# Kernel optimization log

Measured on AMD Instinct MI355X. Metric: run time of the kernel, lower is better.

Reference implementation:

```python
import jax, jax.numpy as jnp
import numpy as np

N_NODES = 100000
N_EDGES = 1600000
D = 128
L = 3
BN_EPS = 1e-5


def setup_inputs() -> dict:
    key = jax.random.key(0)
    ks = jax.random.split(key, 6)
    x = jax.random.normal(ks[0], (N_NODES, D), dtype=jnp.float32)
    edge_index = jax.random.randint(ks[1], (2, N_EDGES), 0, N_NODES, dtype=jnp.int64)
    Wl = jax.random.normal(ks[2], (L, D, D), dtype=jnp.float32) / np.sqrt(D)
    bl = jax.random.normal(ks[3], (L, D), dtype=jnp.float32) * 0.01
    Wr = jax.random.normal(ks[4], (L, D, D), dtype=jnp.float32) / np.sqrt(D)
    gamma = jnp.ones((L, D), dtype=jnp.float32)
    beta = jnp.zeros((L, D), dtype=jnp.float32)
    return {"x": x, "edge_index": edge_index, "Wl": Wl, "bl": bl,
            "Wr": Wr, "gamma": gamma, "beta": beta}


def _sage_layer(x, src, dst, inv_deg, Wl_i, bl_i, Wr_i, gamma_i, beta_i):
    # mean aggregation over incoming edges: scatter-add messages then divide by degree
    agg_sum = jax.ops.segment_sum(x[src], dst, num_segments=N_NODES)  # [N, D]
    agg = agg_sum * inv_deg[:, None]
    # SAGEConv: lin_l(agg) (with bias) + lin_r(x) (no bias)
    h = jnp.einsum('nd,hd->nh', agg, Wl_i) + bl_i + jnp.einsum('nd,hd->nh', x, Wr_i)
    # BatchNorm1d (training-mode batch stats, biased variance)
    mean = jnp.mean(h, axis=0)
    var = jnp.mean(jnp.square(h - mean), axis=0)
    h = (h - mean) * jax.lax.rsqrt(var + BN_EPS) * gamma_i + beta_i
    return jax.nn.relu(h)  # dropout is identity in eval mode


def reference(x, edge_index, Wl, bl, Wr, gamma, beta):
    src, dst = edge_index[0], edge_index[1]
    deg = jax.ops.segment_sum(jnp.ones((N_EDGES,), jnp.float32), dst,
                              num_segments=N_NODES)
    inv_deg = 1.0 / jnp.maximum(deg, 1.0)
    for i in range(L):
        h = _sage_layer(x, src, dst, inv_deg, Wl[i], bl[i], Wr[i], gamma[i], beta[i])
        if 0 < i < L - 1:  # middle layers get a scaled residual (shapes match)
            x = x + 0.5 * h
        else:
            x = h
    return x
```

## Files before the change

kernel.cpp:

```cpp
#include <hip/hip_runtime.h>

#define N_NODES 100000
#define N_EDGES 1600000
#define D 128
#define BN_EPS 1e-5f
#define N_GB ((N_NODES + 63) / 64)
#define NPART 8
#define FILL_BLOCKS 2048
#define NODES_PER_PART (N_NODES / NPART)
#define CAP 80

typedef short bf16x8 __attribute__((ext_vector_type(8)));
typedef float f32x4 __attribute__((ext_vector_type(4)));

__device__ inline unsigned short f32_to_bf16_rne(float f) {
    unsigned u = __builtin_bit_cast(unsigned, f);
    u += 0x7fffu + ((u >> 16) & 1u);
    return (unsigned short)(u >> 16);
}
__device__ inline float bf16lo_to_f32(unsigned v) { return __builtin_bit_cast(float, v << 16); }
__device__ inline float bf16hi_to_f32(unsigned v) { return __builtin_bit_cast(float, v & 0xffff0000u); }

__device__ inline void gload_lds16(const void* g, void* l) {
    __builtin_amdgcn_global_load_lds((const __attribute__((address_space(1))) unsigned*)g,
                                     (__attribute__((address_space(3))) unsigned*)l, 16, 0, 0);
}


__global__ __launch_bounds__(256) void k_prep(const float* __restrict__ x_in,
                                              const float* __restrict__ Wl, const float* __restrict__ Wr,
                                              unsigned short* __restrict__ xhi,
                                              unsigned short* __restrict__ wl_hi, unsigned short* __restrict__ wl_lo,
                                              unsigned short* __restrict__ wr_hi, unsigned short* __restrict__ wr_lo) {
    for (int idx = blockIdx.x * 256 + threadIdx.x; idx < N_NODES * 32; idx += FILL_BLOCKS * 256) {
        float4 v = ((const float4*)x_in)[idx];
        uint2 p;
        p.x = (unsigned)f32_to_bf16_rne(v.x) | ((unsigned)f32_to_bf16_rne(v.y) << 16);
        p.y = (unsigned)f32_to_bf16_rne(v.z) | ((unsigned)f32_to_bf16_rne(v.w) << 16);
        ((uint2*)xhi)[idx] = p;
    }
    for (int i = blockIdx.x * 256 + threadIdx.x; i < 2 * 3 * D * D; i += FILL_BLOCKS * 256) {
        const float* srcp = (i < 3 * D * D) ? Wl : Wr;
        int j = (i < 3 * D * D) ? i : i - 3 * D * D;
        float w = srcp[j];
        unsigned short h = f32_to_bf16_rne(w);
        float rem = w - bf16lo_to_f32((unsigned)h);
        if (i < 3 * D * D) { wl_hi[j] = h; wl_lo[j] = f32_to_bf16_rne(rem); }
        else               { wr_hi[j] = h; wr_lo[j] = f32_to_bf16_rne(rem); }
    }
}

__global__ __launch_bounds__(256) void k_fill(const int* __restrict__ src, const int* __restrict__ dst,
                                              int* __restrict__ cursor, int* __restrict__ colidx) {
    const int part = blockIdx.x & (NPART - 1);
    const int lo = part * NODES_PER_PART;
    const int hi = lo + NODES_PER_PART;
    const int stride = (FILL_BLOCKS / NPART) * 256;
    for (int e = (blockIdx.x >> 3) * 256 + threadIdx.x; e < N_EDGES; e += stride) {
        int d = dst[e];
        if (d >= lo && d < hi) {
            int pos = atomicAdd(&cursor[d], 1);
            if (pos < CAP) colidx[d * CAP + pos] = src[e];
        }
    }
}


__global__ __launch_bounds__(256) void k_agg(const unsigned short* __restrict__ xhi,
                                             const int* __restrict__ cursor, const int* __restrict__ colidx,
                                             unsigned short* __restrict__ agghi) {
    const int wid = threadIdx.x >> 6;
    const int l = threadIdx.x & 63;
    const int n = blockIdx.x * 4 + wid;
    if (n >= N_NODES) return;
    const int degree = cursor[n];
    const int b = n * CAP;
    const int e = b + (degree < CAP ? degree : CAP);
    const int c8 = l & 15;
    const int g = l >> 4;
    const size_t coff = (size_t)c8 * 16;

    float acc[8];
#pragma unroll
    for (int k = 0; k < 8; k++) acc[k] = 0.f;

    int i = b;
    while (i < e) {
        int chunk = e - i; if (chunk > 64) chunk = 64;
        int myE = colidx[i + (l < chunk ? l : chunk - 1)];
        int j = 0;
        for (; j + 8 <= chunk; j += 8) {
            int s0 = __shfl(myE, j + g);
            int s1 = __shfl(myE, j + 4 + g);
            uint4 v0 = *(const uint4*)((const char*)xhi + (size_t)s0 * 256 + coff);
            uint4 v1 = *(const uint4*)((const char*)xhi + (size_t)s1 * 256 + coff);
            acc[0] += bf16lo_to_f32(v0.x); acc[1] += bf16hi_to_f32(v0.x);
            acc[2] += bf16lo_to_f32(v0.y); acc[3] += bf16hi_to_f32(v0.y);
            acc[4] += bf16lo_to_f32(v0.z); acc[5] += bf16hi_to_f32(v0.z);
            acc[6] += bf16lo_to_f32(v0.w); acc[7] += bf16hi_to_f32(v0.w);
            acc[0] += bf16lo_to_f32(v1.x); acc[1] += bf16hi_to_f32(v1.x);
            acc[2] += bf16lo_to_f32(v1.y); acc[3] += bf16hi_to_f32(v1.y);
            acc[4] += bf16lo_to_f32(v1.z); acc[5] += bf16hi_to_f32(v1.z);
            acc[6] += bf16lo_to_f32(v1.w); acc[7] += bf16hi_to_f32(v1.w);
        }
        for (; j + 4 <= chunk; j += 4) {
            int s0 = __shfl(myE, j + g);
            uint4 v0 = *(const uint4*)((const char*)xhi + (size_t)s0 * 256 + coff);
            acc[0] += bf16lo_to_f32(v0.x); acc[1] += bf16hi_to_f32(v0.x);
            acc[2] += bf16lo_to_f32(v0.y); acc[3] += bf16hi_to_f32(v0.y);
            acc[4] += bf16lo_to_f32(v0.z); acc[5] += bf16hi_to_f32(v0.z);
            acc[6] += bf16lo_to_f32(v0.w); acc[7] += bf16hi_to_f32(v0.w);
        }
        if (j < chunk) {
            int idx = j + g;
            int s0 = __shfl(myE, idx < chunk ? idx : chunk - 1);
            if (idx < chunk) {
                uint4 v0 = *(const uint4*)((const char*)xhi + (size_t)s0 * 256 + coff);
                acc[0] += bf16lo_to_f32(v0.x); acc[1] += bf16hi_to_f32(v0.x);
                acc[2] += bf16lo_to_f32(v0.y); acc[3] += bf16hi_to_f32(v0.y);
                acc[4] += bf16lo_to_f32(v0.z); acc[5] += bf16hi_to_f32(v0.z);
                acc[6] += bf16lo_to_f32(v0.w); acc[7] += bf16hi_to_f32(v0.w);
            }
        }
        i += chunk;
    }
#pragma unroll
    for (int k = 0; k < 8; k++) {
        acc[k] += __shfl_xor(acc[k], 16);
        acc[k] += __shfl_xor(acc[k], 32);
    }
    if (g == 0) {
        float idg = 1.0f / fmaxf((float)degree, 1.0f);
        uint4 p;
        p.x = (unsigned)f32_to_bf16_rne(acc[0] * idg) | ((unsigned)f32_to_bf16_rne(acc[1] * idg) << 16);
        p.y = (unsigned)f32_to_bf16_rne(acc[2] * idg) | ((unsigned)f32_to_bf16_rne(acc[3] * idg) << 16);
        p.z = (unsigned)f32_to_bf16_rne(acc[4] * idg) | ((unsigned)f32_to_bf16_rne(acc[5] * idg) << 16);
        p.w = (unsigned)f32_to_bf16_rne(acc[6] * idg) | ((unsigned)f32_to_bf16_rne(acc[7] * idg) << 16);
        *(uint4*)((char*)agghi + (size_t)n * 256 + coff) = p;
    }
}

__global__ __launch_bounds__(256, 2) void k_gemm(
    const unsigned short* __restrict__ agg_hi, const unsigned short* __restrict__ x_hi,
    const unsigned short* __restrict__ wl_hi, const unsigned short* __restrict__ wl_lo,
    const unsigned short* __restrict__ wr_hi, const unsigned short* __restrict__ wr_lo,
    const float* __restrict__ bl, unsigned short* __restrict__ h, float* __restrict__ partial) {
    __shared__ char lds[32768];
    const int t = threadIdx.x;
    const int w = t >> 6;
    const int l = t & 63;
    const int lr = l & 15;
    const int lg = l >> 4;
    const int base = blockIdx.x * 64;
    const int j0 = w * 32;

    {
#pragma unroll
        for (int i = 0; i < 8; i++) {
            int c = w * 8 + i;
            int ci = c & 15;
            int m = ci >> 2, kk = ci & 3;
            int n = base + m * 16 + lr;
            if (n > N_NODES - 1) n = N_NODES - 1;
            size_t goff = (size_t)n * 256 + kk * 64 + lg * 16;
            const char* srcp = ((c & 16) ? (const char*)x_hi : (const char*)agg_hi) + goff;
            gload_lds16(srcp, lds + c * 1024);
        }
    }

    f32x4 acc[4][2];
#pragma unroll
    for (int m = 0; m < 4; m++)
#pragma unroll
        for (int f = 0; f < 2; f++) acc[m][f] = (f32x4){0.f, 0.f, 0.f, 0.f};

#pragma unroll
    for (int seg = 0; seg < 2; seg++) {
        const unsigned short* WH = seg ? wr_hi : wl_hi;
        const unsigned short* WLo = seg ? wr_lo : wl_lo;
        bf16x8 wh[4][2], wlo[4][2];
#pragma unroll
        for (int kk = 0; kk < 4; kk++)
#pragma unroll
            for (int f = 0; f < 2; f++) {
                size_t wo = (size_t)(j0 + f * 16 + lr) * D + kk * 32 + lg * 8;
                wh[kk][f] = *(const bf16x8*)(WH + wo);
                wlo[kk][f] = *(const bf16x8*)(WLo + wo);
            }
        asm volatile("" :: "v"(wh[0][0]), "v"(wh[0][1]), "v"(wh[1][0]), "v"(wh[1][1]),
                           "v"(wh[2][0]), "v"(wh[2][1]), "v"(wh[3][0]), "v"(wh[3][1]));
        asm volatile("" :: "v"(wlo[0][0]), "v"(wlo[0][1]), "v"(wlo[1][0]), "v"(wlo[1][1]),
                           "v"(wlo[2][0]), "v"(wlo[2][1]), "v"(wlo[3][0]), "v"(wlo[3][1]));
        if (seg == 0) __syncthreads();
        const int tb = seg * 16384;
#pragma unroll
        for (int kk = 0; kk < 4; kk++) {
            bf16x8 a[4];
#pragma unroll
            for (int m = 0; m < 4; m++)
                a[m] = *(const bf16x8*)(lds + tb + (m * 4 + kk) * 1024 + l * 16);
#pragma unroll
            for (int f = 0; f < 2; f++)
#pragma unroll
                for (int m = 0; m < 4; m++) {
                    acc[m][f] = __builtin_amdgcn_mfma_f32_16x16x32_bf16(a[m], wh[kk][f], acc[m][f], 0, 0, 0);
                    acc[m][f] = __builtin_amdgcn_mfma_f32_16x16x32_bf16(a[m], wlo[kk][f], acc[m][f], 0, 0, 0);
                }
        }
    }

    float s1[2] = {0.f, 0.f}, s2[2] = {0.f, 0.f};
#pragma unroll
    for (int f = 0; f < 2; f++) {
        const int col = j0 + f * 16 + lr;
        const float bias = bl[col];
#pragma unroll
        for (int m = 0; m < 4; m++) {
#pragma unroll
            for (int r = 0; r < 4; r++) {
                int n = base + m * 16 + lg * 4 + r;
                if (n < N_NODES) {
                    float v = acc[m][f][r] + bias;
                    h[(size_t)n * D + col] = f32_to_bf16_rne(v);
                    s1[f] += v;
                    s2[f] += v * v;
                }
            }
        }
    }
#pragma unroll
    for (int f = 0; f < 2; f++) {
        s1[f] += __shfl_xor(s1[f], 16);
        s1[f] += __shfl_xor(s1[f], 32);
        s2[f] += __shfl_xor(s2[f], 16);
        s2[f] += __shfl_xor(s2[f], 32);
    }
    if (l < 16) {
        float* pp = partial + (size_t)blockIdx.x * 256;
        pp[j0 + l] = s1[0];
        pp[j0 + 16 + l] = s1[1];
        pp[128 + j0 + l] = s2[0];
        pp[128 + j0 + 16 + l] = s2[1];
    }
}

__global__ __launch_bounds__(256) void k_bnred(const float* __restrict__ partial, float* __restrict__ bn32) {
    int t = threadIdx.x;
    float s = 0.f;
    for (int b = blockIdx.x; b < N_GB; b += 32)
        s += partial[(size_t)b * 256 + t];
    bn32[blockIdx.x * 256 + t] = s;
}

__global__ __launch_bounds__(256) void k_apply(const unsigned short* __restrict__ h,
                                               const float* __restrict__ bn32,
                                               const float* __restrict__ gamma, const float* __restrict__ beta,
                                               const unsigned short* __restrict__ xres_hi,
                                               unsigned short* __restrict__ out_hi,
                                               float* __restrict__ out_f32, int mode) {
    __shared__ float sa[128], sc[128];
    int t = threadIdx.x;
    if (t < 128) {
        float m1 = 0.f, m2 = 0.f;
#pragma unroll 8
        for (int i = 0; i < 32; i++) {
            m1 += bn32[i * 256 + t];
            m2 += bn32[i * 256 + 128 + t];
        }
        float mean = m1 * (1.0f / N_NODES);
        float var = m2 * (1.0f / N_NODES) - mean * mean;
        float inv = rsqrtf(var + BN_EPS);
        float av = gamma[t] * inv;
        sa[t] = av;
        sc[t] = beta[t] - mean * av;
    }
    __syncthreads();
    int idx = blockIdx.x * 256 + t;
    if (idx >= N_NODES * 32) return;
    int c0 = (idx & 31) * 4;
    uint2 hv = ((const uint2*)h)[idx];
    float r0 = fmaxf(fmaf(bf16lo_to_f32(hv.x), sa[c0], sc[c0]), 0.f);
    float r1 = fmaxf(fmaf(bf16hi_to_f32(hv.x), sa[c0 + 1], sc[c0 + 1]), 0.f);
    float r2 = fmaxf(fmaf(bf16lo_to_f32(hv.y), sa[c0 + 2], sc[c0 + 2]), 0.f);
    float r3 = fmaxf(fmaf(bf16hi_to_f32(hv.y), sa[c0 + 3], sc[c0 + 3]), 0.f);
    if (mode == 1) {
        uint2 xv = ((const uint2*)xres_hi)[idx];
        r0 = fmaf(0.5f, r0, bf16lo_to_f32(xv.x));
        r1 = fmaf(0.5f, r1, bf16hi_to_f32(xv.x));
        r2 = fmaf(0.5f, r2, bf16lo_to_f32(xv.y));
        r3 = fmaf(0.5f, r3, bf16hi_to_f32(xv.y));
    }
    if (mode == 2) {
        ((float4*)out_f32)[idx] = make_float4(r0, r1, r2, r3);
    } else {
        uint2 p;
        p.x = (unsigned)f32_to_bf16_rne(r0) | ((unsigned)f32_to_bf16_rne(r1) << 16);
        p.y = (unsigned)f32_to_bf16_rne(r2) | ((unsigned)f32_to_bf16_rne(r3) << 16);
        ((uint2*)out_hi)[idx] = p;
    }
}


extern "C" void kernel_launch(void* const* d_in, const int* in_sizes, int n_in,
                              void* d_out, int out_size, void* d_ws, size_t ws_size,
                              hipStream_t stream) {
    const float* x_in = (const float*)d_in[0];
    const int* ei = (const int*)d_in[1];
    const float* Wl = (const float*)d_in[2];
    const float* bl = (const float*)d_in[3];
    const float* Wr = (const float*)d_in[4];
    const float* gamma = (const float*)d_in[5];
    const float* beta = (const float*)d_in[6];
    float* out = (float*)d_out;

    char* ws = (char*)d_ws;
    unsigned short* xhiA = (unsigned short*)ws; ws += (size_t)N_NODES * D * 2;
    unsigned short* xhiB = (unsigned short*)ws; ws += (size_t)N_NODES * D * 2;
    unsigned short* agghi = (unsigned short*)ws; ws += (size_t)N_NODES * D * 2;
    int* cursor = (int*)ws; ws += (size_t)N_NODES * 4;
    int* colidx = (int*)ws; ws += (size_t)N_NODES * CAP * 4;
    unsigned short* wl_hi = (unsigned short*)ws; ws += (size_t)3 * D * D * 2;
    unsigned short* wl_lo = (unsigned short*)ws; ws += (size_t)3 * D * D * 2;
    unsigned short* wr_hi = (unsigned short*)ws; ws += (size_t)3 * D * D * 2;
    unsigned short* wr_lo = (unsigned short*)ws; ws += (size_t)3 * D * D * 2;
    float* partial = (float*)ws; ws += (size_t)N_GB * 256 * 4;
    float* bn32 = (float*)ws; ws += 32 * 256 * 4;

    const int* src = ei;
    const int* dst = ei + N_EDGES;

    hipMemsetAsync(cursor, 0, (size_t)N_NODES * 4, stream);
    k_prep<<<FILL_BLOCKS, 256, 0, stream>>>(x_in, Wl, Wr, xhiA, wl_hi, wl_lo, wr_hi, wr_lo);
    k_fill<<<FILL_BLOCKS, 256, 0, stream>>>(src, dst, cursor, colidx);

    unsigned short* xin[3] = { xhiA, xhiB, xhiA };
    unsigned short* xout[3] = { xhiB, xhiA, (unsigned short*)0 };
    int mode[3] = { 0, 1, 2 };

    for (int i = 0; i < 3; i++) {
        k_agg<<<(N_NODES + 3) / 4, 256, 0, stream>>>(xin[i], cursor, colidx, agghi);
        k_gemm<<<N_GB, 256, 0, stream>>>(agghi, xin[i],
                                         wl_hi + (size_t)i * D * D, wl_lo + (size_t)i * D * D,
                                         wr_hi + (size_t)i * D * D, wr_lo + (size_t)i * D * D,
                                         bl + (size_t)i * D, agghi, partial);
        k_bnred<<<32, 256, 0, stream>>>(partial, bn32);
        k_apply<<<(N_NODES * 32 + 255) / 256, 256, 0, stream>>>(agghi, bn32,
                                                                gamma + (size_t)i * D, beta + (size_t)i * D,
                                                                xin[i], xout[i], out, mode[i]);
    }
}
```

Before: 504.2 us.

## Gather neighbor features in FP8, fuse fill/prep, single-block BN reduction

Each layer output is now also stored as an FP8 copy, and the aggregation kernel gathers neighbor rows from it, halving the bytes per random-access row load compared with bf16. The CSR fill and the input/weight conversion are merged into one launch with separate block ranges, which removes a kernel launch and lets the two overlap. The BN statistics reduction moves into a single 1024-thread block that also computes the scale/shift coefficients, so k_apply no longer re-reduces 32 partials per block. The risk is accuracy loss from FP8 quantization of the aggregated features, plus an extra FP8 store in k_apply and a serial single-block reduction.

```diff
diff --git a/kernel.cpp b/kernel.cpp
--- a/kernel.cpp
+++ b/kernel.cpp
@@ -7,11 +7,13 @@
 #define N_GB ((N_NODES + 63) / 64)
 #define NPART 8
 #define FILL_BLOCKS 2048
+#define CONV_BLOCKS 512
 #define NODES_PER_PART (N_NODES / NPART)
 #define CAP 80
 
 typedef short bf16x8 __attribute__((ext_vector_type(8)));
 typedef float f32x4 __attribute__((ext_vector_type(4)));
+typedef float f32x2 __attribute__((ext_vector_type(2)));
 
 __device__ inline unsigned short f32_to_bf16_rne(float f) {
     unsigned u = __builtin_bit_cast(unsigned, f);
@@ -26,20 +28,44 @@
                                      (__attribute__((address_space(3))) unsigned*)l, 16, 0, 0);
 }
 
-
-__global__ __launch_bounds__(256) void k_prep(const float* __restrict__ x_in,
-                                              const float* __restrict__ Wl, const float* __restrict__ Wr,
-                                              unsigned short* __restrict__ xhi,
-                                              unsigned short* __restrict__ wl_hi, unsigned short* __restrict__ wl_lo,
-                                              unsigned short* __restrict__ wr_hi, unsigned short* __restrict__ wr_lo) {
-    for (int idx = blockIdx.x * 256 + threadIdx.x; idx < N_NODES * 32; idx += FILL_BLOCKS * 256) {
+__device__ inline unsigned pack_fp8x4(float a, float b, float c, float d) {
+    int q = 0;
+    q = __builtin_amdgcn_cvt_pk_fp8_f32(a, b, q, false);
+    q = __builtin_amdgcn_cvt_pk_fp8_f32(c, d, q, true);
+    return (unsigned)q;
+}
+
+__global__ __launch_bounds__(256) void k_fillprep(
+    const int* __restrict__ src, const int* __restrict__ dst,
+    int* __restrict__ cursor, int* __restrict__ colidx,
+    const float* __restrict__ x_in, const float* __restrict__ Wl, const float* __restrict__ Wr,
+    unsigned short* __restrict__ xhi, unsigned* __restrict__ xq8,
+    unsigned short* __restrict__ wl_hi, unsigned short* __restrict__ wl_lo,
+    unsigned short* __restrict__ wr_hi, unsigned short* __restrict__ wr_lo) {
+    if (blockIdx.x < FILL_BLOCKS) {
+        const int part = blockIdx.x & (NPART - 1);
+        const int lo = part * NODES_PER_PART;
+        const int hi = lo + NODES_PER_PART;
+        const int stride = (FILL_BLOCKS / NPART) * 256;
+        for (int e = (blockIdx.x >> 3) * 256 + threadIdx.x; e < N_EDGES; e += stride) {
+            int d = dst[e];
+            if (d >= lo && d < hi) {
+                int pos = atomicAdd(&cursor[d], 1);
+                if (pos < CAP) colidx[d * CAP + pos] = src[e];
+            }
+        }
+        return;
+    }
+    const int bb = blockIdx.x - FILL_BLOCKS;
+    for (int idx = bb * 256 + threadIdx.x; idx < N_NODES * 32; idx += CONV_BLOCKS * 256) {
         float4 v = ((const float4*)x_in)[idx];
         uint2 p;
         p.x = (unsigned)f32_to_bf16_rne(v.x) | ((unsigned)f32_to_bf16_rne(v.y) << 16);
         p.y = (unsigned)f32_to_bf16_rne(v.z) | ((unsigned)f32_to_bf16_rne(v.w) << 16);
         ((uint2*)xhi)[idx] = p;
-    }
-    for (int i = blockIdx.x * 256 + threadIdx.x; i < 2 * 3 * D * D; i += FILL_BLOCKS * 256) {
+        xq8[idx] = pack_fp8x4(v.x, v.y, v.z, v.w);
+    }
+    for (int i = bb * 256 + threadIdx.x; i < 2 * 3 * D * D; i += CONV_BLOCKS * 256) {
         const float* srcp = (i < 3 * D * D) ? Wl : Wr;
         int j = (i < 3 * D * D) ? i : i - 3 * D * D;
         float w = srcp[j];
@@ -50,23 +76,8 @@
     }
 }
 
-__global__ __launch_bounds__(256) void k_fill(const int* __restrict__ src, const int* __restrict__ dst,
-                                              int* __restrict__ cursor, int* __restrict__ colidx) {
-    const int part = blockIdx.x & (NPART - 1);
-    const int lo = part * NODES_PER_PART;
-    const int hi = lo + NODES_PER_PART;
-    const int stride = (FILL_BLOCKS / NPART) * 256;
-    for (int e = (blockIdx.x >> 3) * 256 + threadIdx.x; e < N_EDGES; e += stride) {
-        int d = dst[e];
-        if (d >= lo && d < hi) {
-            int pos = atomicAdd(&cursor[d], 1);
-            if (pos < CAP) colidx[d * CAP + pos] = src[e];
-        }
-    }
-}
-
-
-__global__ __launch_bounds__(256) void k_agg(const unsigned short* __restrict__ xhi,
+
+__global__ __launch_bounds__(256) void k_agg(const unsigned char* __restrict__ xq8,
                                              const int* __restrict__ cursor, const int* __restrict__ colidx,
                                              unsigned short* __restrict__ agghi) {
     const int wid = threadIdx.x >> 6;
@@ -78,11 +89,21 @@
     const int e = b + (degree < CAP ? degree : CAP);
     const int c8 = l & 15;
     const int g = l >> 4;
-    const size_t coff = (size_t)c8 * 16;
+    const size_t coff8 = (size_t)c8 * 8;
 
     float acc[8];
 #pragma unroll
     for (int k = 0; k < 8; k++) acc[k] = 0.f;
+
+#define ACC_ROW(vv)                                                             \
+    {                                                                           \
+        f32x2 a0 = __builtin_amdgcn_cvt_pk_f32_fp8((vv).x, false);              \
+        f32x2 a1 = __builtin_amdgcn_cvt_pk_f32_fp8((vv).x, true);               \
+        f32x2 a2 = __builtin_amdgcn_cvt_pk_f32_fp8((vv).y, false);              \
+        f32x2 a3 = __builtin_amdgcn_cvt_pk_f32_fp8((vv).y, true);               \
+        acc[0] += a0[0]; acc[1] += a0[1]; acc[2] += a1[0]; acc[3] += a1[1];     \
+        acc[4] += a2[0]; acc[5] += a2[1]; acc[6] += a3[0]; acc[7] += a3[1];     \
+    }
 
     int i = b;
     while (i < e) {
@@ -92,38 +113,27 @@
         for (; j + 8 <= chunk; j += 8) {
             int s0 = __shfl(myE, j + g);
             int s1 = __shfl(myE, j + 4 + g);
-            uint4 v0 = *(const uint4*)((const char*)xhi + (size_t)s0 * 256 + coff);
-            uint4 v1 = *(const uint4*)((const char*)xhi + (size_t)s1 * 256 + coff);
-            acc[0] += bf16lo_to_f32(v0.x); acc[1] += bf16hi_to_f32(v0.x);
-            acc[2] += bf16lo_to_f32(v0.y); acc[3] += bf16hi_to_f32(v0.y);
-            acc[4] += bf16lo_to_f32(v0.z); acc[5] += bf16hi_to_f32(v0.z);
-            acc[6] += bf16lo_to_f32(v0.w); acc[7] += bf16hi_to_f32(v0.w);
-            acc[0] += bf16lo_to_f32(v1.x); acc[1] += bf16hi_to_f32(v1.x);
-            acc[2] += bf16lo_to_f32(v1.y); acc[3] += bf16hi_to_f32(v1.y);
-            acc[4] += bf16lo_to_f32(v1.z); acc[5] += bf16hi_to_f32(v1.z);
-            acc[6] += bf16lo_to_f32(v1.w); acc[7] += bf16hi_to_f32(v1.w);
+            uint2 v0 = *(const uint2*)(xq8 + (size_t)s0 * 128 + coff8);
+            uint2 v1 = *(const uint2*)(xq8 + (size_t)s1 * 128 + coff8);
+            ACC_ROW(v0);
+            ACC_ROW(v1);
         }
         for (; j + 4 <= chunk; j += 4) {
             int s0 = __shfl(myE, j + g);
-            uint4 v0 = *(const uint4*)((const char*)xhi + (size_t)s0 * 256 + coff);
-            acc[0] += bf16lo_to_f32(v0.x); acc[1] += bf16hi_to_f32(v0.x);
-            acc[2] += bf16lo_to_f32(v0.y); acc[3] += bf16hi_to_f32(v0.y);
-            acc[4] += bf16lo_to_f32(v0.z); acc[5] += bf16hi_to_f32(v0.z);
-            acc[6] += bf16lo_to_f32(v0.w); acc[7] += bf16hi_to_f32(v0.w);
+            uint2 v0 = *(const uint2*)(xq8 + (size_t)s0 * 128 + coff8);
+            ACC_ROW(v0);
         }
         if (j < chunk) {
             int idx = j + g;
             int s0 = __shfl(myE, idx < chunk ? idx : chunk - 1);
             if (idx < chunk) {
-                uint4 v0 = *(const uint4*)((const char*)xhi + (size_t)s0 * 256 + coff);
-                acc[0] += bf16lo_to_f32(v0.x); acc[1] += bf16hi_to_f32(v0.x);
-                acc[2] += bf16lo_to_f32(v0.y); acc[3] += bf16hi_to_f32(v0.y);
-                acc[4] += bf16lo_to_f32(v0.z); acc[5] += bf16hi_to_f32(v0.z);
-                acc[6] += bf16lo_to_f32(v0.w); acc[7] += bf16hi_to_f32(v0.w);
+                uint2 v0 = *(const uint2*)(xq8 + (size_t)s0 * 128 + coff8);
+                ACC_ROW(v0);
             }
         }
         i += chunk;
     }
+#undef ACC_ROW
 #pragma unroll
     for (int k = 0; k < 8; k++) {
         acc[k] += __shfl_xor(acc[k], 16);
@@ -136,7 +146,7 @@
         p.y = (unsigned)f32_to_bf16_rne(acc[2] * idg) | ((unsigned)f32_to_bf16_rne(acc[3] * idg) << 16);
         p.z = (unsigned)f32_to_bf16_rne(acc[4] * idg) | ((unsigned)f32_to_bf16_rne(acc[5] * idg) << 16);
         p.w = (unsigned)f32_to_bf16_rne(acc[6] * idg) | ((unsigned)f32_to_bf16_rne(acc[7] * idg) << 16);
-        *(uint4*)((char*)agghi + (size_t)n * 256 + coff) = p;
+        *(uint4*)((char*)agghi + (size_t)n * 256 + (size_t)c8 * 16) = p;
     }
 }
 
@@ -244,35 +254,42 @@
     }
 }
 
-__global__ __launch_bounds__(256) void k_bnred(const float* __restrict__ partial, float* __restrict__ bn32) {
-    int t = threadIdx.x;
+__global__ __launch_bounds__(1024) void k_bnred(const float* __restrict__ partial,
+                                                const float* __restrict__ gamma, const float* __restrict__ beta,
+                                                float* __restrict__ coef) {
+    __shared__ float red[4][256];
+    __shared__ float tot[256];
+    const int t = threadIdx.x;
+    const int c = t & 255;
+    const int g = t >> 8;
     float s = 0.f;
-    for (int b = blockIdx.x; b < N_GB; b += 32)
-        s += partial[(size_t)b * 256 + t];
-    bn32[blockIdx.x * 256 + t] = s;
+    for (int b = g; b < N_GB; b += 4)
+        s += partial[(size_t)b * 256 + c];
+    red[g][c] = s;
+    __syncthreads();
+    if (t < 256) tot[t] = red[0][t] + red[1][t] + red[2][t] + red[3][t];
+    __syncthreads();
+    if (t < 128) {
+        float mean = tot[t] * (1.0f / N_NODES);
+        float var = tot[128 + t] * (1.0f / N_NODES) - mean * mean;
+        float inv = rsqrtf(var + BN_EPS);
+        float av = gamma[t] * inv;
+        coef[t] = av;
+        coef[128 + t] = beta[t] - mean * av;
+    }
 }
 
 __global__ __launch_bounds__(256) void k_apply(const unsigned short* __restrict__ h,
-                                               const float* __restrict__ bn32,
-                                               const float* __restrict__ gamma, const float* __restrict__ beta,
+                                               const float* __restrict__ coef,
                                                const unsigned short* __restrict__ xres_hi,
                                                unsigned short* __restrict__ out_hi,
+                                               unsigned* __restrict__ out_q8,
                                                float* __restrict__ out_f32, int mode) {
     __shared__ float sa[128], sc[128];
     int t = threadIdx.x;
     if (t < 128) {
-        float m1 = 0.f, m2 = 0.f;
-#pragma unroll 8
-        for (int i = 0; i < 32; i++) {
-            m1 += bn32[i * 256 + t];
-            m2 += bn32[i * 256 + 128 + t];
-        }
-        float mean = m1 * (1.0f / N_NODES);
-        float var = m2 * (1.0f / N_NODES) - mean * mean;
-        float inv = rsqrtf(var + BN_EPS);
-        float av = gamma[t] * inv;
-        sa[t] = av;
-        sc[t] = beta[t] - mean * av;
+        sa[t] = coef[t];
+        sc[t] = coef[128 + t];
     }
     __syncthreads();
     int idx = blockIdx.x * 256 + t;
@@ -297,6 +314,7 @@
         p.x = (unsigned)f32_to_bf16_rne(r0) | ((unsigned)f32_to_bf16_rne(r1) << 16);
         p.y = (unsigned)f32_to_bf16_rne(r2) | ((unsigned)f32_to_bf16_rne(r3) << 16);
         ((uint2*)out_hi)[idx] = p;
+        out_q8[idx] = pack_fp8x4(r0, r1, r2, r3);
     }
 }
 
@@ -317,6 +335,8 @@
     unsigned short* xhiA = (unsigned short*)ws; ws += (size_t)N_NODES * D * 2;
     unsigned short* xhiB = (unsigned short*)ws; ws += (size_t)N_NODES * D * 2;
     unsigned short* agghi = (unsigned short*)ws; ws += (size_t)N_NODES * D * 2;
+    unsigned* xq8A = (unsigned*)ws; ws += (size_t)N_NODES * D;
+    unsigned* xq8B = (unsigned*)ws; ws += (size_t)N_NODES * D;
     int* cursor = (int*)ws; ws += (size_t)N_NODES * 4;
     int* colidx = (int*)ws; ws += (size_t)N_NODES * CAP * 4;
     unsigned short* wl_hi = (unsigned short*)ws; ws += (size_t)3 * D * D * 2;
@@ -324,28 +344,31 @@
     unsigned short* wr_hi = (unsigned short*)ws; ws += (size_t)3 * D * D * 2;
     unsigned short* wr_lo = (unsigned short*)ws; ws += (size_t)3 * D * D * 2;
     float* partial = (float*)ws; ws += (size_t)N_GB * 256 * 4;
-    float* bn32 = (float*)ws; ws += 32 * 256 * 4;
+    float* coef = (float*)ws; ws += 256 * 4;
 
     const int* src = ei;
     const int* dst = ei + N_EDGES;
 
     hipMemsetAsync(cursor, 0, (size_t)N_NODES * 4, stream);
-    k_prep<<<FILL_BLOCKS, 256, 0, stream>>>(x_in, Wl, Wr, xhiA, wl_hi, wl_lo, wr_hi, wr_lo);
-    k_fill<<<FILL_BLOCKS, 256, 0, stream>>>(src, dst, cursor, colidx);
-
-    unsigned short* xin[3] = { xhiA, xhiB, xhiA };
-    unsigned short* xout[3] = { xhiB, xhiA, (unsigned short*)0 };
+    k_fillprep<<<FILL_BLOCKS + CONV_BLOCKS, 256, 0, stream>>>(src, dst, cursor, colidx,
+                                                              x_in, Wl, Wr, xhiA, xq8A,
+                                                              wl_hi, wl_lo, wr_hi, wr_lo);
+
+    unsigned short* xin_hi[3] = { xhiA, xhiB, xhiA };
+    unsigned* xin_q8[3] = { xq8A, xq8B, xq8A };
+    unsigned short* xout_hi[3] = { xhiB, xhiA, (unsigned short*)0 };
+    unsigned* xout_q8[3] = { xq8B, xq8A, (unsigned*)0 };
     int mode[3] = { 0, 1, 2 };
 
     for (int i = 0; i < 3; i++) {
-        k_agg<<<(N_NODES + 3) / 4, 256, 0, stream>>>(xin[i], cursor, colidx, agghi);
-        k_gemm<<<N_GB, 256, 0, stream>>>(agghi, xin[i],
+        k_agg<<<(N_NODES + 3) / 4, 256, 0, stream>>>((const unsigned char*)xin_q8[i], cursor, colidx, agghi);
+        k_gemm<<<N_GB, 256, 0, stream>>>(agghi, xin_hi[i],
                                          wl_hi + (size_t)i * D * D, wl_lo + (size_t)i * D * D,
                                          wr_hi + (size_t)i * D * D, wr_lo + (size_t)i * D * D,
                                          bl + (size_t)i * D, agghi, partial);
-        k_bnred<<<32, 256, 0, stream>>>(partial, bn32);
-        k_apply<<<(N_NODES * 32 + 255) / 256, 256, 0, stream>>>(agghi, bn32,
-                                                                gamma + (size_t)i * D, beta + (size_t)i * D,
-                                                                xin[i], xout[i], out, mode[i]);
-    }
-}
+        k_bnred<<<1, 1024, 0, stream>>>(partial, gamma + (size_t)i * D, beta + (size_t)i * D, coef);
+        k_apply<<<(N_NODES * 32 + 255) / 256, 256, 0, stream>>>(agghi, coef,
+                                                                xin_hi[i], xout_hi[i], xout_q8[i],
+                                                                out, mode[i]);
+    }
+}
```

Measured after the change: 703.3 us. 1.39x slower.
